# Kernel tuning notes

Measured on AMD Instinct MI355X. Metric: run time of the kernel, lower is better.

The kernel has to match this reference:

```python
import jax, jax.numpy as jnp
import numpy as np

B, N, D, H = 128, 32768, 768, 16
DH = D // H          # per-head hidden_size = memory_dim // num_heads = 48
BETA = 0.25          # scaling (inverse temperature)
STEPS = 5            # update_steps_max
TOPK = 4


def _ln(x, g, b):
    # torch nn.LayerNorm over last dim (biased variance, eps=1e-5), affine
    m = jnp.mean(x, axis=-1, keepdims=True)
    v = jnp.var(x, axis=-1, keepdims=True)
    return (x - m) * jax.lax.rsqrt(v + 1e-5) * g + b


def _l2norm(x):
    # F.normalize(x, dim=-1): x / max(||x||, 1e-12)
    n = jnp.linalg.norm(x, axis=-1, keepdims=True)
    return x / jnp.maximum(n, 1e-12)


def setup_inputs() -> dict:
    key = jax.random.key(0)
    ks = jax.random.split(key, 8)
    s = 0.05  # weight init scale to keep activations sane
    return {
        "query_embedding": jax.random.normal(ks[0], (B, D), jnp.float32),
        "memory_bank": jax.random.normal(ks[1], (N, D), jnp.float32),
        "ln_k_g": jnp.ones((D,), jnp.float32), "ln_k_b": jnp.zeros((D,), jnp.float32),
        "ln_q_g": jnp.ones((D,), jnp.float32), "ln_q_b": jnp.zeros((D,), jnp.float32),
        "ln_v_g": jnp.ones((D,), jnp.float32), "ln_v_b": jnp.zeros((D,), jnp.float32),
        "Wq": jax.random.normal(ks[2], (D, D), jnp.float32) * s, "bq": jnp.zeros((D,), jnp.float32),
        "Wk": jax.random.normal(ks[3], (D, D), jnp.float32) * s, "bk": jnp.zeros((D,), jnp.float32),
        "Wv": jax.random.normal(ks[4], (D, D), jnp.float32) * s, "bv": jnp.zeros((D,), jnp.float32),
        "Wo": jax.random.normal(ks[5], (D, D), jnp.float32) * s, "bo": jnp.zeros((D,), jnp.float32),
        "W1": jax.random.normal(ks[6], (D, D), jnp.float32) * s, "b1": jnp.zeros((D,), jnp.float32),
        "W2": jax.random.normal(ks[7], (D, D), jnp.float32) * s, "b2": jnp.zeros((D,), jnp.float32),
    }


def reference(query_embedding, memory_bank, ln_k_g, ln_k_b, ln_q_g, ln_q_b,
              ln_v_g, ln_v_b, Wq, bq, Wk, bk, Wv, bv, Wo, bo, W1, b1, W2, b2):
    # Affine LayerNorms on stored pattern, state pattern, pattern projection.
    # memory_bank is shared across the batch, so normalize/project it ONCE
    # instead of materializing the (B, N, D) expand from the torch code.
    stored = _ln(memory_bank, ln_k_g, ln_k_b)        # (N, D)
    state = _ln(query_embedding, ln_q_g, ln_q_b)     # (B, D) -- state pattern, seq len 1
    projp = _ln(memory_bank, ln_v_g, ln_v_b)         # (N, D)

    k = (stored @ Wk.T + bk).reshape(N, H, DH)       # (N, H, dh)
    v = (projp @ Wv.T + bv).reshape(N, H, DH)        # (N, H, dh)
    q = (state @ Wq.T + bq).reshape(B, H, DH)        # (B, H, dh)

    # Hopfield convergence: xi <- softmax(beta * xi K^T) K, repeated STEPS times
    def step(xi, _):
        attn = jax.nn.softmax(BETA * jnp.einsum('bhd,nhd->bhn', xi, k), axis=-1)
        return jnp.einsum('bhn,nhd->bhd', attn, k), None

    xi, _ = jax.lax.scan(step, q, None, length=STEPS)

    # Final readout against the (separately normalized) pattern projection V
    attn = jax.nn.softmax(BETA * jnp.einsum('bhd,nhd->bhn', xi, k), axis=-1)  # (B, H, N)
    converged = jnp.einsum('bhn,nhd->bhd', attn, v).reshape(B, D) @ Wo.T + bo  # (B, D)

    # Retrieval head: residual + MLP + cosine-sim logits + top-k
    combined = query_embedding + converged
    rq = jax.nn.relu(combined @ W1.T + b1) @ W2.T + b2
    logits = (_l2norm(rq) @ _l2norm(memory_bank).T) * 20.0   # (B, N)
    top_indices = jax.lax.top_k(logits, TOPK)[1]              # (B, TOPK)
    return top_indices, logits
```

## Files before the change

kernel.cpp:

```cpp
#include <hip/hip_runtime.h>
#include <math.h>

#define NTOT 32768
#define DMODEL 768
#define BSZ 128
#define NHEAD 16
#define DH 48
#define BETA 0.25f

typedef _Float16 f16;
typedef f16 f16x8 __attribute__((ext_vector_type(8)));
typedef f16 f16x4 __attribute__((ext_vector_type(4)));
typedef float f32x4 __attribute__((ext_vector_type(4)));

__global__ __launch_bounds__(256)
void row_stats(const float* __restrict__ X, int M, float* __restrict__ mean,
               float* __restrict__ rstd, float* __restrict__ l2inv) {
  const int row = blockIdx.x * 4 + (threadIdx.x >> 6);
  const int lane = threadIdx.x & 63;
  if (row >= M) return;
  const float* x = X + (size_t)row * DMODEL;
  float s = 0.f, s2 = 0.f;
  for (int i = lane; i < DMODEL; i += 64) {
    float v = x[i];
    s += v; s2 += v * v;
  }
#pragma unroll
  for (int off = 32; off; off >>= 1) {
    s  += __shfl_xor(s, off);
    s2 += __shfl_xor(s2, off);
  }
  if (lane == 0) {
    float mu = s * (1.f / DMODEL);
    float var = s2 * (1.f / DMODEL) - mu * mu;
    mean[row] = mu;
    rstd[row] = rsqrtf(var + 1e-5f);
    if (l2inv) l2inv[row] = 1.f / fmaxf(sqrtf(s2), 1e-12f);
  }
}

__global__ __launch_bounds__(256)
void stats_norm_mb(const float* __restrict__ mb, f16* __restrict__ nh_hi,
                   f16* __restrict__ nh_lo, float* __restrict__ c1,
                   float* __restrict__ c2) {
  const int row = blockIdx.x * 4 + (threadIdx.x >> 6);
  const int lane = threadIdx.x & 63;
  const float* x = mb + (size_t)row * DMODEL;
  float v[12];
  float s = 0.f, s2 = 0.f;
#pragma unroll
  for (int j = 0; j < 3; j++) {
    const float4 v4 = *(const float4*)(x + lane * 4 + j * 256);
    v[j * 4 + 0] = v4.x; v[j * 4 + 1] = v4.y;
    v[j * 4 + 2] = v4.z; v[j * 4 + 3] = v4.w;
    s += v4.x + v4.y + v4.z + v4.w;
    s2 += v4.x * v4.x + v4.y * v4.y + v4.z * v4.z + v4.w * v4.w;
  }
#pragma unroll
  for (int off = 32; off; off >>= 1) {
    s  += __shfl_xor(s, off);
    s2 += __shfl_xor(s2, off);
  }
  const float mu = s * (1.f / DMODEL);
  const float var = s2 * (1.f / DMODEL) - mu * mu;
  const float istd = sqrtf(var + 1e-5f);
  const float rs = 1.f / istd;
  f16* oh = nh_hi + (size_t)row * DMODEL;
  f16* ol = nh_lo + (size_t)row * DMODEL;
#pragma unroll
  for (int j = 0; j < 3; j++) {
    f16x4 h4, l4;
#pragma unroll
    for (int q = 0; q < 4; q++) {
      const float sv = (v[j * 4 + q] - mu) * rs;
      const f16 h = (f16)sv;
      h4[q] = h;
      l4[q] = (f16)(sv - (float)h);
    }
    *(f16x4*)(oh + lane * 4 + j * 256) = h4;
    *(f16x4*)(ol + lane * 4 + j * 256) = l4;
  }
  if (lane == 0) {
    const float l2i = 1.f / fmaxf(sqrtf(s2), 1e-12f);
    c1[row] = 20.f * l2i * istd;
    c2[row] = 20.f * l2i * mu;
  }
}

__global__ __launch_bounds__(256)
void rq_prep(const float* __restrict__ rq, f16* __restrict__ hi,
             f16* __restrict__ lo, float* __restrict__ ainv,
             float* __restrict__ rqsum) {
  const int row = blockIdx.x * 4 + (threadIdx.x >> 6);
  const int lane = threadIdx.x & 63;
  const float* x = rq + (size_t)row * DMODEL;
  f16* oh = hi + (size_t)row * DMODEL;
  f16* ol = lo + (size_t)row * DMODEL;
  float s = 0.f, s2 = 0.f;
#pragma unroll
  for (int j = 0; j < 3; j++) {
    const int d = lane * 4 + j * 256;
    const float4 v4 = *(const float4*)(x + d);
    const float vv[4] = {v4.x, v4.y, v4.z, v4.w};
    f16x4 h4, l4;
#pragma unroll
    for (int q = 0; q < 4; q++) {
      s += vv[q]; s2 += vv[q] * vv[q];
      const f16 h = (f16)vv[q];
      h4[q] = h;
      l4[q] = (f16)(vv[q] - (float)h);
    }
    *(f16x4*)(oh + d) = h4;
    *(f16x4*)(ol + d) = l4;
  }
#pragma unroll
  for (int off = 32; off; off >>= 1) {
    s  += __shfl_xor(s, off);
    s2 += __shfl_xor(s2, off);
  }
  if (lane == 0) {
    rqsum[row] = s;
    ainv[row] = 1.f / fmaxf(sqrtf(s2), 1e-12f);
  }
}

__global__ __launch_bounds__(256)
void prep_w(const float* __restrict__ Wk, const float* __restrict__ bk,
            const float* __restrict__ gk, const float* __restrict__ blnk,
            const float* __restrict__ Wv, const float* __restrict__ bv,
            const float* __restrict__ gv, const float* __restrict__ blnv,
            f16* __restrict__ Wc_hi, f16* __restrict__ Wc_lo,
            float* __restrict__ biasc) {
  const int o = blockIdx.x * 4 + (threadIdx.x >> 6);
  const int lane = threadIdx.x & 63;
  const bool isK = o < DMODEL;
  const float* W = isK ? (Wk + (size_t)o * DMODEL)
                       : (Wv + (size_t)(o - DMODEL) * DMODEL);
  const float* g   = isK ? gk : gv;
  const float* bln = isK ? blnk : blnv;
  float bacc = 0.f;
  for (int d = lane * 4; d < DMODEL; d += 256) {
    const float4 wv = *(const float4*)(W + d);
    const float4 g4 = *(const float4*)(g + d);
    const float4 b4 = *(const float4*)(bln + d);
    bacc += wv.x * b4.x + wv.y * b4.y + wv.z * b4.z + wv.w * b4.w;
    const float sv[4] = {wv.x * g4.x * 16.f, wv.y * g4.y * 16.f,
                         wv.z * g4.z * 16.f, wv.w * g4.w * 16.f};
    f16x4 h4, l4;
#pragma unroll
    for (int j = 0; j < 4; j++) {
      const f16 h = (f16)sv[j];
      h4[j] = h;
      l4[j] = (f16)(sv[j] - (float)h);
    }
    *(f16x4*)(Wc_hi + (size_t)o * DMODEL + d) = h4;
    *(f16x4*)(Wc_lo + (size_t)o * DMODEL + d) = l4;
  }
#pragma unroll
  for (int off = 32; off; off >>= 1) bacc += __shfl_xor(bacc, off);
  if (lane == 0) biasc[o] = (isK ? bk[o] : bv[o - DMODEL]) + bacc;
}

__global__ __launch_bounds__(256)
void proj_mfma(const f16* __restrict__ nh_hi, const f16* __restrict__ nh_lo,
               const f16* __restrict__ Wc_hi, const f16* __restrict__ Wc_lo,
               const float* __restrict__ biasc,
               f16* __restrict__ k_hi, f16* __restrict__ k_lo,
               f16* __restrict__ T_hi, f16* __restrict__ T_lo, int oc0) {
  __shared__ __align__(16) f16 As[128][64];
  __shared__ __align__(16) f16 Bs[128][64];
  const int t = threadIdx.x;
  const int n0 = oc0 + blockIdx.x * 128;
  const int m0 = blockIdx.y * 128;
  const int w = t >> 6, lane = t & 63;
  const int l15 = lane & 15, lq = lane >> 4;
  const int wm = w >> 1, wn = w & 1;
  const int sc = (lane & 7) ^ (lane >> 3);
  const int srow = lane >> 3;

  f32x4 acc[4][4];
#pragma unroll
  for (int a = 0; a < 4; a++)
#pragma unroll
    for (int b = 0; b < 4; b++)
#pragma unroll
      for (int r = 0; r < 4; r++) acc[a][b][r] = 0.f;

  for (int k0 = 0; k0 < DMODEL; k0 += 32) {
    __syncthreads();
#pragma unroll
    for (int i = 0; i < 4; i++) {
      const int rb = (w * 4 + i) * 8;
      const f16* asrc = ((sc < 4) ? nh_hi : nh_lo) +
          (size_t)(m0 + rb + srow) * DMODEL + k0 + (sc & 3) * 8;
      __builtin_amdgcn_global_load_lds(
          (__attribute__((address_space(1))) void*)asrc,
          (__attribute__((address_space(3))) void*)&As[rb][0], 16, 0, 0);
      const f16* bsrc = ((sc < 4) ? Wc_hi : Wc_lo) +
          (size_t)(n0 + rb + srow) * DMODEL + k0 + (sc & 3) * 8;
      __builtin_amdgcn_global_load_lds(
          (__attribute__((address_space(1))) void*)bsrc,
          (__attribute__((address_space(3))) void*)&Bs[rb][0], 16, 0, 0);
    }
    __syncthreads();

    f16x8 nhh[4], nhl[4];
#pragma unroll
    for (int fm = 0; fm < 4; fm++) {
      const int row = wm * 64 + fm * 16 + l15;
      const int e = row & 7;
      nhh[fm] = *(const f16x8*)&As[row][(lq ^ e) * 8];
      nhl[fm] = *(const f16x8*)&As[row][((lq + 4) ^ e) * 8];
    }
    f16x8 wh[4], wl[4];
#pragma unroll
    for (int fo = 0; fo < 4; fo++) {
      const int row = wn * 64 + fo * 16 + l15;
      const int e = row & 7;
      wh[fo] = *(const f16x8*)&Bs[row][(lq ^ e) * 8];
      wl[fo] = *(const f16x8*)&Bs[row][((lq + 4) ^ e) * 8];
    }
#pragma unroll
    for (int fo = 0; fo < 4; fo++)
#pragma unroll
      for (int fm = 0; fm < 4; fm++) {
        f32x4 a = acc[fo][fm];
        a = __builtin_amdgcn_mfma_f32_16x16x32_f16(wh[fo], nhh[fm], a, 0, 0, 0);
        a = __builtin_amdgcn_mfma_f32_16x16x32_f16(wh[fo], nhl[fm], a, 0, 0, 0);
        a = __builtin_amdgcn_mfma_f32_16x16x32_f16(wl[fo], nhh[fm], a, 0, 0, 0);
        acc[fo][fm] = a;
      }
  }
  const int oc = n0 + wn * 64;
  const int obase = (oc - oc0) + lq * 4;
  const bool wantRow = (oc0 == 0);
#pragma unroll
  for (int fo = 0; fo < 4; fo++) {
    const float4 bb = *(const float4*)(biasc + oc + fo * 16 + lq * 4);
    const float bbv[4] = {bb.x, bb.y, bb.z, bb.w};
    const int o = obase + fo * 16;
#pragma unroll
    for (int fm = 0; fm < 4; fm++) {
      const int mrow = m0 + wm * 64 + fm * 16 + l15;
      f16x4 h4, l4;
#pragma unroll
      for (int r = 0; r < 4; r++) {
        const float v = acc[fo][fm][r] * 0.0625f + bbv[r];
        const f16 h = (f16)v;
        h4[r] = h;
        l4[r] = (f16)(v - (float)h);
      }
      if (wantRow) {
        const size_t moff = (size_t)mrow * DMODEL + o;
        *(f16x4*)(k_hi + moff) = h4;
        *(f16x4*)(k_lo + moff) = l4;
      }
#pragma unroll
      for (int r = 0; r < 4; r++) {
        T_hi[(size_t)(o + r) * NTOT + mrow] = h4[r];
        T_lo[(size_t)(o + r) * NTOT + mrow] = l4[r];
      }
    }
  }
}

__global__ __launch_bounds__(256)
void logits_mfma(const f16* __restrict__ nh_hi, const f16* __restrict__ nh_lo,
                 const f16* __restrict__ rq_hi, const f16* __restrict__ rq_lo,
                 const float* __restrict__ c1, const float* __restrict__ c2,
                 const float* __restrict__ ainv, const float* __restrict__ rqsum,
                 float* __restrict__ out) {
  __shared__ __align__(16) f16 As[128][64];
  __shared__ __align__(16) f16 Bs[128][64];
  const int t = threadIdx.x;
  const int n0 = blockIdx.x * 128;
  const int w = t >> 6, lane = t & 63;
  const int l15 = lane & 15, lq = lane >> 4;
  const int wm = w >> 1, wn = w & 1;
  const int sc = (lane & 7) ^ (lane >> 3);
  const int srow = lane >> 3;

  f32x4 acc[4][4];
#pragma unroll
  for (int a = 0; a < 4; a++)
#pragma unroll
    for (int b = 0; b < 4; b++)
#pragma unroll
      for (int r = 0; r < 4; r++) acc[a][b][r] = 0.f;

  for (int k0 = 0; k0 < DMODEL; k0 += 32) {
    __syncthreads();
#pragma unroll
    for (int i = 0; i < 4; i++) {
      const int rb = (w * 4 + i) * 8;
      const f16* asrc = ((sc < 4) ? nh_hi : nh_lo) +
          (size_t)(n0 + rb + srow) * DMODEL + k0 + (sc & 3) * 8;
      __builtin_amdgcn_global_load_lds(
          (__attribute__((address_space(1))) void*)asrc,
          (__attribute__((address_space(3))) void*)&As[rb][0], 16, 0, 0);
      const f16* bsrc = ((sc < 4) ? rq_hi : rq_lo) +
          (size_t)(rb + srow) * DMODEL + k0 + (sc & 3) * 8;
      __builtin_amdgcn_global_load_lds(
          (__attribute__((address_space(1))) void*)bsrc,
          (__attribute__((address_space(3))) void*)&Bs[rb][0], 16, 0, 0);
    }
    __syncthreads();

    f16x8 ah[4], al[4];
#pragma unroll
    for (int fo = 0; fo < 4; fo++) {
      const int row = wn * 64 + fo * 16 + l15;
      const int e = row & 7;
      ah[fo] = *(const f16x8*)&As[row][(lq ^ e) * 8];
      al[fo] = *(const f16x8*)&As[row][((lq + 4) ^ e) * 8];
    }
    f16x8 bh[4], bl[4];
#pragma unroll
    for (int fm = 0; fm < 4; fm++) {
      const int row = wm * 64 + fm * 16 + l15;
      const int e = row & 7;
      bh[fm] = *(const f16x8*)&Bs[row][(lq ^ e) * 8];
      bl[fm] = *(const f16x8*)&Bs[row][((lq + 4) ^ e) * 8];
    }
#pragma unroll
    for (int fo = 0; fo < 4; fo++)
#pragma unroll
      for (int fm = 0; fm < 4; fm++) {
        f32x4 a = acc[fo][fm];
        a = __builtin_amdgcn_mfma_f32_16x16x32_f16(ah[fo], bh[fm], a, 0, 0, 0);
        a = __builtin_amdgcn_mfma_f32_16x16x32_f16(ah[fo], bl[fm], a, 0, 0, 0);
        a = __builtin_amdgcn_mfma_f32_16x16x32_f16(al[fo], bh[fm], a, 0, 0, 0);
        acc[fo][fm] = a;
      }
  }
#pragma unroll
  for (int fm = 0; fm < 4; fm++) {
    const int b = wm * 64 + fm * 16 + l15;
    const float am = ainv[b];
    const float rs = rqsum[b];
#pragma unroll
    for (int fo = 0; fo < 4; fo++) {
      const int nb = n0 + wn * 64 + fo * 16 + lq * 4;
      const float4 c1v = *(const float4*)(c1 + nb);
      const float4 c2v = *(const float4*)(c2 + nb);
      const float c1a[4] = {c1v.x, c1v.y, c1v.z, c1v.w};
      const float c2a[4] = {c2v.x, c2v.y, c2v.z, c2v.w};
      float4 o4;
      float ov[4];
#pragma unroll
      for (int r = 0; r < 4; r++)
        ov[r] = am * (acc[fo][fm][r] * c1a[r] + rs * c2a[r]);
      o4.x = ov[0]; o4.y = ov[1]; o4.z = ov[2]; o4.w = ov[3];
      *(float4*)(out + (size_t)b * NTOT + nb) = o4;
    }
  }
}

__global__ __launch_bounds__(256)
void ln_gemm_f32(const float* __restrict__ A, const float* __restrict__ mean,
                 const float* __restrict__ rstd, const float* __restrict__ g,
                 const float* __restrict__ bln, const float* __restrict__ W,
                 const float* __restrict__ bias, float* __restrict__ out) {
  __shared__ float As[16][68];
  __shared__ float Ws[16][68];
  const int t = threadIdx.x;
  const int m0 = blockIdx.y << 6, n0 = blockIdx.x << 6;
  const int tm = t >> 4, tn = t & 15;
  const int lr = t >> 2;
  const int lk = (t & 3) << 2;
  const float muL = mean[m0 + lr];
  const float rsL = rstd[m0 + lr];
  float acc[4][4] = {};
  for (int k0 = 0; k0 < DMODEL; k0 += 16) {
    float4 a4 = *(const float4*)(A + (size_t)(m0 + lr) * DMODEL + k0 + lk);
    float4 g4 = *(const float4*)(g + k0 + lk);
    float4 b4 = *(const float4*)(bln + k0 + lk);
    As[lk + 0][lr] = (a4.x - muL) * rsL * g4.x + b4.x;
    As[lk + 1][lr] = (a4.y - muL) * rsL * g4.y + b4.y;
    As[lk + 2][lr] = (a4.z - muL) * rsL * g4.z + b4.z;
    As[lk + 3][lr] = (a4.w - muL) * rsL * g4.w + b4.w;
    float4 w4 = *(const float4*)(W + (size_t)(n0 + lr) * DMODEL + k0 + lk);
    Ws[lk + 0][lr] = w4.x;
    Ws[lk + 1][lr] = w4.y;
    Ws[lk + 2][lr] = w4.z;
    Ws[lk + 3][lr] = w4.w;
    __syncthreads();
#pragma unroll
    for (int kk = 0; kk < 16; kk++) {
      const float4 av = *(const float4*)(&As[kk][tm * 4]);
      const float4 bv = *(const float4*)(&Ws[kk][tn * 4]);
      const float a[4] = {av.x, av.y, av.z, av.w};
      const float b[4] = {bv.x, bv.y, bv.z, bv.w};
#pragma unroll
      for (int i = 0; i < 4; i++)
#pragma unroll
        for (int j = 0; j < 4; j++) acc[i][j] += a[i] * b[j];
    }
    __syncthreads();
  }
  const float4 bia = *(const float4*)(bias + n0 + tn * 4);
  const float bb[4] = {bia.x, bia.y, bia.z, bia.w};
#pragma unroll
  for (int i = 0; i < 4; i++) {
    const int m = m0 + tm * 4 + i;
    float4 o4;
    o4.x = acc[i][0] + bb[0];
    o4.y = acc[i][1] + bb[1];
    o4.z = acc[i][2] + bb[2];
    o4.w = acc[i][3] + bb[3];
    *(float4*)(out + (size_t)m * DMODEL + n0 + tn * 4) = o4;
  }
}

__global__ __launch_bounds__(256)
void gemm_bias(const float* __restrict__ A, const float* __restrict__ W,
               const float* __restrict__ bias, const float* __restrict__ add,
               float* __restrict__ out, int relu) {
  __shared__ float As[16][68];
  __shared__ float Ws[16][68];
  const int t = threadIdx.x;
  const int m0 = blockIdx.y << 6, n0 = blockIdx.x << 6;
  const int tm = t >> 4, tn = t & 15;
  const int lr = t >> 2;
  const int lk = (t & 3) << 2;
  float acc[4][4] = {};
  for (int k0 = 0; k0 < DMODEL; k0 += 16) {
    float4 a4 = *(const float4*)(A + (size_t)(m0 + lr) * DMODEL + k0 + lk);
    As[lk + 0][lr] = a4.x;
    As[lk + 1][lr] = a4.y;
    As[lk + 2][lr] = a4.z;
    As[lk + 3][lr] = a4.w;
    float4 w4 = *(const float4*)(W + (size_t)(n0 + lr) * DMODEL + k0 + lk);
    Ws[lk + 0][lr] = w4.x;
    Ws[lk + 1][lr] = w4.y;
    Ws[lk + 2][lr] = w4.z;
    Ws[lk + 3][lr] = w4.w;
    __syncthreads();
#pragma unroll
    for (int kk = 0; kk < 16; kk++) {
      const float4 av = *(const float4*)(&As[kk][tm * 4]);
      const float4 bv = *(const float4*)(&Ws[kk][tn * 4]);
      const float a[4] = {av.x, av.y, av.z, av.w};
      const float b[4] = {bv.x, bv.y, bv.z, bv.w};
#pragma unroll
      for (int i = 0; i < 4; i++)
#pragma unroll
        for (int j = 0; j < 4; j++) acc[i][j] += a[i] * b[j];
    }
    __syncthreads();
  }
  const float4 bia = *(const float4*)(bias + n0 + tn * 4);
  const float bb[4] = {bia.x, bia.y, bia.z, bia.w};
#pragma unroll
  for (int i = 0; i < 4; i++) {
    const int m = m0 + tm * 4 + i;
    float v[4];
#pragma unroll
    for (int j = 0; j < 4; j++) v[j] = acc[i][j] + bb[j];
    if (add) {
      const float4 a4 = *(const float4*)(add + (size_t)m * DMODEL + n0 + tn * 4);
      v[0] += a4.x; v[1] += a4.y; v[2] += a4.z; v[3] += a4.w;
    }
    if (relu) {
#pragma unroll
      for (int j = 0; j < 4; j++) v[j] = fmaxf(v[j], 0.f);
    }
    float4 o4 = {v[0], v[1], v[2], v[3]};
    *(float4*)(out + (size_t)m * DMODEL + n0 + tn * 4) = o4;
  }
}

__global__ __launch_bounds__(256)
void split_xi_k(const float* __restrict__ xi, f16* __restrict__ hi,
                f16* __restrict__ lo) {
  const int i = blockIdx.x * 256 + threadIdx.x;
  float4 v = ((const float4*)xi)[i];
  float s[4] = {v.x * BETA, v.y * BETA, v.z * BETA, v.w * BETA};
  f16x4 h4, l4;
#pragma unroll
  for (int j = 0; j < 4; j++) {
    f16 h = (f16)s[j];
    h4[j] = h;
    l4[j] = (f16)(s[j] - (float)h);
  }
  ((f16x4*)hi)[i] = h4;
  ((f16x4*)lo)[i] = l4;
}

#define FCHUNK 64
#define FROWS (NTOT / FCHUNK)

__global__ __launch_bounds__(256)
void flash_round(const f16* __restrict__ k_hi, const f16* __restrict__ k_lo,
                 const f16* __restrict__ pvT_hi, const f16* __restrict__ pvT_lo,
                 const f16* __restrict__ xi_hi, const f16* __restrict__ xi_lo,
                 float* __restrict__ part_ml, float* __restrict__ part_o) {
  const int h = blockIdx.y, chunk = blockIdx.x;
  const int tid = threadIdx.x, w = tid >> 6, lane = tid & 63;
  const int l15 = lane & 15, lq = lane >> 4;
  const int b0 = w * 32;

  __shared__ __align__(16) f16 krow[2][32][56];
  __shared__ __align__(16) f16 ptT[2][48][40];
  __shared__ __align__(16) f16 pHi[4][32][40];
  __shared__ __align__(16) f16 pLo[4][32][40];

  const int nbase = chunk * FROWS;

  const f16* ssrc[3];
  f16* sdst[3];
  int sstep[3];
#pragma unroll
  for (int cc = 0; cc < 3; cc++) {
    const int idx = cc * 256 + tid;
    if (idx < 384) {
      const int tsel = idx / 192, q = idx % 192;
      const int r = q / 6, c = q % 6;
      ssrc[cc] = (tsel ? k_lo : k_hi) + (size_t)(nbase + r) * DMODEL + h * DH + c * 8;
      sdst[cc] = &krow[tsel][r][c * 8];
      sstep[cc] = 32 * DMODEL;
    } else {
      const int j = idx - 384;
      const int tsel = j / 192, q = j % 192;
      const int d = q / 4, c = q % 4;
      ssrc[cc] = (tsel ? pvT_lo : pvT_hi) + (size_t)(h * DH + d) * NTOT + nbase + c * 8;
      sdst[cc] = &ptT[tsel][d][c * 8];
      sstep[cc] = 32;
    }
  }

  const f16x8 zf = {};
  f16x8 xqh[2][2], xql[2][2];
#pragma unroll
  for (int bt = 0; bt < 2; bt++) {
    const size_t xoff = (size_t)(b0 + bt * 16 + l15) * DMODEL + h * DH;
    xqh[bt][0] = *(const f16x8*)(xi_hi + xoff + lq * 8);
    xql[bt][0] = *(const f16x8*)(xi_lo + xoff + lq * 8);
    const size_t xo1 = xoff + 32 + (lq & 1) * 8;
    f16x8 th = *(const f16x8*)(xi_hi + xo1);
    f16x8 tl = *(const f16x8*)(xi_lo + xo1);
    xqh[bt][1] = (lq < 2) ? th : zf;
    xql[bt][1] = (lq < 2) ? tl : zf;
  }

  float m[2] = {-1e30f, -1e30f}, lsum[2] = {0.f, 0.f};
  f32x4 O[3][2];
#pragma unroll
  for (int mt = 0; mt < 3; mt++)
#pragma unroll
    for (int bt = 0; bt < 2; bt++)
#pragma unroll
      for (int j = 0; j < 4; j++) O[mt][bt][j] = 0.f;

  f16x8 stg[3];
#pragma unroll
  for (int cc = 0; cc < 3; cc++) {
    stg[cc] = *(const f16x8*)ssrc[cc];
    ssrc[cc] += sstep[cc];
  }
#pragma unroll
  for (int cc = 0; cc < 3; cc++) *(f16x8*)sdst[cc] = stg[cc];
  __syncthreads();

  for (int it = 0; it < 16; it++) {
    if (it < 15) {
#pragma unroll
      for (int cc = 0; cc < 3; cc++) {
        stg[cc] = *(const f16x8*)ssrc[cc];
        ssrc[cc] += sstep[cc];
      }
    }

    f16x8 akh[2][2], akl[2][2];
#pragma unroll
    for (int nt = 0; nt < 2; nt++) {
      const int row = nt * 16 + l15;
      akh[nt][0] = *(const f16x8*)&krow[0][row][lq * 8];
      akl[nt][0] = *(const f16x8*)&krow[1][row][lq * 8];
      f16x8 t0 = *(const f16x8*)&krow[0][row][32 + (lq & 1) * 8];
      f16x8 t1 = *(const f16x8*)&krow[1][row][32 + (lq & 1) * 8];
      akh[nt][1] = (lq < 2) ? t0 : zf;
      akl[nt][1] = (lq < 2) ? t1 : zf;
    }
    f32x4 S[2][2];
#pragma unroll
    for (int nt = 0; nt < 2; nt++)
#pragma unroll
      for (int bt = 0; bt < 2; bt++) {
        f32x4 s = {};
        s = __builtin_amdgcn_mfma_f32_16x16x32_f16(akh[nt][0], xqh[bt][0], s, 0, 0, 0);
        s = __builtin_amdgcn_mfma_f32_16x16x32_f16(akh[nt][1], xqh[bt][1], s, 0, 0, 0);
        s = __builtin_amdgcn_mfma_f32_16x16x32_f16(akh[nt][0], xql[bt][0], s, 0, 0, 0);
        s = __builtin_amdgcn_mfma_f32_16x16x32_f16(akh[nt][1], xql[bt][1], s, 0, 0, 0);
        s = __builtin_amdgcn_mfma_f32_16x16x32_f16(akl[nt][0], xqh[bt][0], s, 0, 0, 0);
        s = __builtin_amdgcn_mfma_f32_16x16x32_f16(akl[nt][1], xqh[bt][1], s, 0, 0, 0);
        S[nt][bt] = s;
      }
    float sc[2];
#pragma unroll
    for (int bt = 0; bt < 2; bt++) {
      float mx = S[0][bt][0];
#pragma unroll
      for (int r = 1; r < 4; r++) mx = fmaxf(mx, S[0][bt][r]);
#pragma unroll
      for (int r = 0; r < 4; r++) mx = fmaxf(mx, S[1][bt][r]);
      mx = fmaxf(mx, __shfl_xor(mx, 16));
      mx = fmaxf(mx, __shfl_xor(mx, 32));
      const float mnew = fmaxf(m[bt], mx);
      sc[bt] = __expf(m[bt] - mnew);
      float ps = 0.f;
#pragma unroll
      for (int nt = 0; nt < 2; nt++) {
        f16x4 ph, pl;
#pragma unroll
        for (int r = 0; r < 4; r++) {
          const float p = __expf(S[nt][bt][r] - mnew);
          ps += p;
          const f16 hh = (f16)p;
          ph[r] = hh;
          pl[r] = (f16)(p - (float)hh);
        }
        *(f16x4*)&pHi[w][bt * 16 + l15][nt * 16 + lq * 4] = ph;
        *(f16x4*)&pLo[w][bt * 16 + l15][nt * 16 + lq * 4] = pl;
      }
      ps += __shfl_xor(ps, 16);
      ps += __shfl_xor(ps, 32);
      lsum[bt] = lsum[bt] * sc[bt] + ps;
      m[bt] = mnew;
    }
    __asm__ volatile("s_waitcnt lgkmcnt(0)" ::: "memory");
    f16x8 avh[3], avl[3];
#pragma unroll
    for (int mt = 0; mt < 3; mt++) {
      avh[mt] = *(const f16x8*)&ptT[0][mt * 16 + l15][lq * 8];
      avl[mt] = *(const f16x8*)&ptT[1][mt * 16 + l15][lq * 8];
    }
    f16x8 pbh[2], pbl[2];
#pragma unroll
    for (int bt = 0; bt < 2; bt++) {
      pbh[bt] = *(const f16x8*)&pHi[w][bt * 16 + l15][lq * 8];
      pbl[bt] = *(const f16x8*)&pLo[w][bt * 16 + l15][lq * 8];
    }
#pragma unroll
    for (int mt = 0; mt < 3; mt++)
#pragma unroll
      for (int bt = 0; bt < 2; bt++) {
#pragma unroll
        for (int j = 0; j < 4; j++) O[mt][bt][j] *= sc[bt];
        f32x4 o = O[mt][bt];
        o = __builtin_amdgcn_mfma_f32_16x16x32_f16(avh[mt], pbh[bt], o, 0, 0, 0);
        o = __builtin_amdgcn_mfma_f32_16x16x32_f16(avh[mt], pbl[bt], o, 0, 0, 0);
        o = __builtin_amdgcn_mfma_f32_16x16x32_f16(avl[mt], pbh[bt], o, 0, 0, 0);
        O[mt][bt] = o;
      }

    if (it < 15) {
      __syncthreads();
#pragma unroll
      for (int cc = 0; cc < 3; cc++) *(f16x8*)sdst[cc] = stg[cc];
      __syncthreads();
    }
  }
  const int pc = h * FCHUNK + chunk;
  if (lq == 0) {
#pragma unroll
    for (int bt = 0; bt < 2; bt++) {
      float* pm = part_ml + ((size_t)pc * BSZ + b0 + bt * 16 + l15) * 2;
      pm[0] = m[bt];
      pm[1] = lsum[bt];
    }
  }
#pragma unroll
  for (int mt = 0; mt < 3; mt++)
#pragma unroll
    for (int bt = 0; bt < 2; bt++) {
      float* po = part_o + ((size_t)pc * BSZ + b0 + bt * 16 + l15) * 48 +
                  mt * 16 + lq * 4;
      *(f32x4*)po = O[mt][bt];
    }
}

__global__ __launch_bounds__(64)
void hopfield_combine(const float* __restrict__ part_ml,
                      const float* __restrict__ part_o, float* __restrict__ dst) {
  const int bh = blockIdx.x;
  const int h = bh >> 7, b = bh & 127;
  const int c = threadIdx.x;
  __shared__ float w[64];
  const float* pm = part_ml + ((size_t)(h * 64 + c) * BSZ + b) * 2;
  const float mp = pm[0];
  const float lp = pm[1];
  float M = mp;
#pragma unroll
  for (int off = 32; off; off >>= 1) M = fmaxf(M, __shfl_xor(M, off));
  const float wp = __expf(mp - M);
  w[c] = wp;
  float L = lp * wp;
#pragma unroll
  for (int off = 32; off; off >>= 1) L += __shfl_xor(L, off);
  __syncthreads();
  if (c < DH) {
    float o = 0.f;
    for (int p = 0; p < 64; p++)
      o += part_o[((size_t)(h * 64 + p) * BSZ + b) * 48 + c] * w[p];
    dst[(size_t)b * DMODEL + h * DH + c] = o / L;
  }
}

__global__ __launch_bounds__(256)
void topk_kernel(const float* __restrict__ logits, float* __restrict__ outIdx) {
  const int b = blockIdx.x;
  const int t = threadIdx.x;
  const float* row = logits + (size_t)b * NTOT;
  float v[4] = {-1e30f, -1e30f, -1e30f, -1e30f};
  int id[4] = {0x7fffffff, 0x7fffffff, 0x7fffffff, 0x7fffffff};
  for (int n = t; n < NTOT; n += 256) {
    const float x = row[n];
    if (x > v[3]) {
      v[3] = x; id[3] = n;
#pragma unroll
      for (int s = 3; s > 0; s--) {
        const bool sw = (v[s] > v[s - 1]) || (v[s] == v[s - 1] && id[s] < id[s - 1]);
        if (sw) {
          float tv = v[s]; v[s] = v[s - 1]; v[s - 1] = tv;
          int ti = id[s]; id[s] = id[s - 1]; id[s - 1] = ti;
        }
      }
    }
  }
  __shared__ float sv[256][4];
  __shared__ int si[256][4];
#pragma unroll
  for (int j = 0; j < 4; j++) { sv[t][j] = v[j]; si[t][j] = id[j]; }
  for (int str = 128; str >= 1; str >>= 1) {
    __syncthreads();
    if (t < str) {
      float a[4], c[4];
      int ai[4], ci[4];
#pragma unroll
      for (int j = 0; j < 4; j++) {
        a[j] = sv[t][j]; ai[j] = si[t][j];
        c[j] = sv[t + str][j]; ci[j] = si[t + str][j];
      }
      float rv[4]; int ri[4];
      int p = 0, q = 0;
#pragma unroll
      for (int oo = 0; oo < 4; oo++) {
        const bool ta = (a[p] > c[q]) || (a[p] == c[q] && ai[p] < ci[q]);
        if (ta) { rv[oo] = a[p]; ri[oo] = ai[p]; p++; }
        else    { rv[oo] = c[q]; ri[oo] = ci[q]; q++; }
      }
#pragma unroll
      for (int j = 0; j < 4; j++) { sv[t][j] = rv[j]; si[t][j] = ri[j]; }
    }
  }
  if (t == 0) {
#pragma unroll
    for (int j = 0; j < 4; j++) outIdx[b * 4 + j] = (float)si[0][j];
  }
}

extern "C" void kernel_launch(void* const* d_in, const int* in_sizes, int n_in,
                              void* d_out, int out_size, void* d_ws, size_t ws_size,
                              hipStream_t stream) {
  const float* qe    = (const float*)d_in[0];
  const float* mb    = (const float*)d_in[1];
  const float* ln_kg = (const float*)d_in[2];
  const float* ln_kb = (const float*)d_in[3];
  const float* ln_qg = (const float*)d_in[4];
  const float* ln_qb = (const float*)d_in[5];
  const float* ln_vg = (const float*)d_in[6];
  const float* ln_vb = (const float*)d_in[7];
  const float* Wq = (const float*)d_in[8];
  const float* bq = (const float*)d_in[9];
  const float* Wk = (const float*)d_in[10];
  const float* bk = (const float*)d_in[11];
  const float* Wv = (const float*)d_in[12];
  const float* bv = (const float*)d_in[13];
  const float* Wo = (const float*)d_in[14];
  const float* bo = (const float*)d_in[15];
  const float* W1 = (const float*)d_in[16];
  const float* b1 = (const float*)d_in[17];
  const float* W2 = (const float*)d_in[18];
  const float* b2 = (const float*)d_in[19];

  float* out = (float*)d_out;
  float* logits = out + BSZ * 4;

  float* ws = (float*)d_ws;
  size_t off = 0;
  auto alloc = [&](size_t n) { float* p = ws + off; off += n; return p; };
  const size_t ND2 = (size_t)NTOT * DMODEL / 2;
  float* c1      = alloc(NTOT);
  float* c2      = alloc(NTOT);
  float* q_mean  = alloc(128);
  float* q_rstd  = alloc(128);
  float* rq_inv  = alloc(128);
  float* rq_sum  = alloc(128);
  float* pad_    = alloc(256);
  f16* k_hi  = (f16*)alloc(ND2);
  f16* k_lo  = (f16*)alloc(ND2);
  f16* T_hi  = (f16*)alloc(ND2);
  f16* T_lo  = (f16*)alloc(ND2);
  f16* nh_hi = (f16*)alloc(ND2);
  f16* nh_lo = (f16*)alloc(ND2);
  float* part_ml = alloc((size_t)NHEAD * FCHUNK * BSZ * 2);
  float* part_o  = alloc((size_t)NHEAD * FCHUNK * BSZ * 48);
  float* xi   = alloc((size_t)BSZ * DMODEL);
  float* conv = alloc((size_t)BSZ * DMODEL);
  float* comb = alloc((size_t)BSZ * DMODEL);
  float* h1   = alloc((size_t)BSZ * DMODEL);
  f16* xi_hi = (f16*)alloc((size_t)BSZ * DMODEL / 2);
  f16* xi_lo = (f16*)alloc((size_t)BSZ * DMODEL / 2);
  f16* rq_hi = (f16*)alloc((size_t)BSZ * DMODEL / 2);
  f16* rq_lo = (f16*)alloc((size_t)BSZ * DMODEL / 2);
  f16* Wc_hi = (f16*)alloc((size_t)2 * DMODEL * DMODEL / 2);
  f16* Wc_lo = (f16*)alloc((size_t)2 * DMODEL * DMODEL / 2);
  float* biasc = alloc(2 * DMODEL);
  (void)ws_size; (void)in_sizes; (void)n_in; (void)out_size; (void)pad_;

  row_stats<<<BSZ / 4, 256, 0, stream>>>(qe, BSZ, q_mean, q_rstd, nullptr);
  stats_norm_mb<<<NTOT / 4, 256, 0, stream>>>(mb, nh_hi, nh_lo, c1, c2);
  prep_w<<<2 * DMODEL / 4, 256, 0, stream>>>(Wk, bk, ln_kg, ln_kb,
                                             Wv, bv, ln_vg, ln_vb,
                                             Wc_hi, Wc_lo, biasc);

  proj_mfma<<<dim3(DMODEL / 128, NTOT / 128), 256, 0, stream>>>(
      nh_hi, nh_lo, Wc_hi, Wc_lo, biasc, k_hi, k_lo, T_hi, T_lo, 0);
  ln_gemm_f32<<<dim3(DMODEL / 64, BSZ / 64), 256, 0, stream>>>(
      qe, q_mean, q_rstd, ln_qg, ln_qb, Wq, bq, xi);

  for (int r = 0; r < 5; r++) {
    split_xi_k<<<96, 256, 0, stream>>>(xi, xi_hi, xi_lo);
    flash_round<<<dim3(FCHUNK, NHEAD), 256, 0, stream>>>(
        k_hi, k_lo, T_hi, T_lo, xi_hi, xi_lo, part_ml, part_o);
    hopfield_combine<<<BSZ * NHEAD, 64, 0, stream>>>(part_ml, part_o, xi);
  }

  proj_mfma<<<dim3(DMODEL / 128, NTOT / 128), 256, 0, stream>>>(
      nh_hi, nh_lo, Wc_hi, Wc_lo, biasc, k_hi, k_lo, T_hi, T_lo, DMODEL);

  split_xi_k<<<96, 256, 0, stream>>>(xi, xi_hi, xi_lo);
  flash_round<<<dim3(FCHUNK, NHEAD), 256, 0, stream>>>(
      k_hi, k_lo, T_hi, T_lo, xi_hi, xi_lo, part_ml, part_o);
  hopfield_combine<<<BSZ * NHEAD, 64, 0, stream>>>(part_ml, part_o, conv);

  gemm_bias<<<dim3(DMODEL / 64, BSZ / 64), 256, 0, stream>>>(conv, Wo, bo, qe, comb, 0);
  gemm_bias<<<dim3(DMODEL / 64, BSZ / 64), 256, 0, stream>>>(comb, W1, b1, nullptr, h1, 1);
  float* rq = conv;
  gemm_bias<<<dim3(DMODEL / 64, BSZ / 64), 256, 0, stream>>>(h1, W2, b2, nullptr, rq, 0);

  rq_prep<<<BSZ / 4, 256, 0, stream>>>(rq, rq_hi, rq_lo, rq_inv, rq_sum);
  logits_mfma<<<NTOT / 128, 256, 0, stream>>>(nh_hi, nh_lo, rq_hi, rq_lo,
                                              c1, c2, rq_inv, rq_sum, logits);

  topk_kernel<<<BSZ, 256, 0, stream>>>(logits, out);
}
```

Measured before the change: 1.309 ms.

## Double-buffer flash tiles via direct global-to-LDS loads and swizzle proj grid

The flash_round kernel now stages K and transposed-V tiles with global_load_lds straight into a double-buffered LDS region. This removes the register round-trip and one barrier per iteration, and lets the next tile's load overlap compute. The V tile uses an XOR swizzle on the LDS layout to avoid bank conflicts, since padding is no longer possible. proj_mfma also remaps workgroup IDs with an 8-way swizzle for better L2 locality. LDS usage grows and correctness depends on load completion ordering at the single remaining barrier.

```diff
diff --git a/kernel.cpp b/kernel.cpp
--- a/kernel.cpp
+++ b/kernel.cpp
@@ -170,8 +170,12 @@
   __shared__ __align__(16) f16 As[128][64];
   __shared__ __align__(16) f16 Bs[128][64];
   const int t = threadIdx.x;
-  const int n0 = oc0 + blockIdx.x * 128;
-  const int m0 = blockIdx.y * 128;
+  const int nwg = gridDim.x * gridDim.y;
+  const int bid = blockIdx.x + blockIdx.y * gridDim.x;
+  const int swz = (bid & 7) * (nwg >> 3) + (bid >> 3);
+  const int bx = swz % gridDim.x, by = swz / gridDim.x;
+  const int n0 = oc0 + bx * 128;
+  const int m0 = by * 128;
   const int w = t >> 6, lane = t & 63;
   const int l15 = lane & 15, lq = lane >> 4;
   const int wm = w >> 1, wn = w & 1;
@@ -500,32 +504,30 @@
   const int l15 = lane & 15, lq = lane >> 4;
   const int b0 = w * 32;
 
-  __shared__ __align__(16) f16 krow[2][32][56];
-  __shared__ __align__(16) f16 ptT[2][48][40];
+  __shared__ __align__(16) f16 stage[2][6144];
   __shared__ __align__(16) f16 pHi[4][32][40];
   __shared__ __align__(16) f16 pLo[4][32][40];
 
   const int nbase = chunk * FROWS;
 
-  const f16* ssrc[3];
-  f16* sdst[3];
-  int sstep[3];
-#pragma unroll
-  for (int cc = 0; cc < 3; cc++) {
-    const int idx = cc * 256 + tid;
-    if (idx < 384) {
-      const int tsel = idx / 192, q = idx % 192;
-      const int r = q / 6, c = q % 6;
-      ssrc[cc] = (tsel ? k_lo : k_hi) + (size_t)(nbase + r) * DMODEL + h * DH + c * 8;
-      sdst[cc] = &krow[tsel][r][c * 8];
-      sstep[cc] = 32 * DMODEL;
+  const f16* gsrc[3];
+  int gstep[3];
+#pragma unroll
+  for (int g = 0; g < 3; g++) {
+    const int s = w * 3 + g;
+    const int ci = s * 64 + lane;
+    if (s < 6) {
+      const int tsel = ci / 192, rem = ci % 192;
+      const int r = rem / 6, dc = rem % 6;
+      gsrc[g] = (tsel ? k_lo : k_hi) + (size_t)(nbase + r) * DMODEL + h * DH + dc * 8;
+      gstep[g] = 32 * DMODEL;
     } else {
-      const int j = idx - 384;
-      const int tsel = j / 192, q = j % 192;
-      const int d = q / 4, c = q % 4;
-      ssrc[cc] = (tsel ? pvT_lo : pvT_hi) + (size_t)(h * DH + d) * NTOT + nbase + c * 8;
-      sdst[cc] = &ptT[tsel][d][c * 8];
-      sstep[cc] = 32;
+      const int j = ci - 384;
+      const int tsel = j / 192, rem = j % 192;
+      const int d = rem / 4, pc = rem % 4;
+      const int nc = pc ^ (d & 3);
+      gsrc[g] = (tsel ? pvT_lo : pvT_hi) + (size_t)(h * DH + d) * NTOT + nbase + nc * 8;
+      gstep[g] = 32;
     }
   }
 
@@ -552,33 +554,38 @@
 #pragma unroll
       for (int j = 0; j < 4; j++) O[mt][bt][j] = 0.f;
 
-  f16x8 stg[3];
-#pragma unroll
-  for (int cc = 0; cc < 3; cc++) {
-    stg[cc] = *(const f16x8*)ssrc[cc];
-    ssrc[cc] += sstep[cc];
-  }
-#pragma unroll
-  for (int cc = 0; cc < 3; cc++) *(f16x8*)sdst[cc] = stg[cc];
+#pragma unroll
+  for (int g = 0; g < 3; g++) {
+    __builtin_amdgcn_global_load_lds(
+        (__attribute__((address_space(1))) void*)gsrc[g],
+        (__attribute__((address_space(3))) void*)&stage[0][(w * 3 + g) * 512],
+        16, 0, 0);
+    gsrc[g] += gstep[g];
+  }
   __syncthreads();
 
+  int cur = 0;
   for (int it = 0; it < 16; it++) {
     if (it < 15) {
 #pragma unroll
-      for (int cc = 0; cc < 3; cc++) {
-        stg[cc] = *(const f16x8*)ssrc[cc];
-        ssrc[cc] += sstep[cc];
-      }
-    }
+      for (int g = 0; g < 3; g++) {
+        __builtin_amdgcn_global_load_lds(
+            (__attribute__((address_space(1))) void*)gsrc[g],
+            (__attribute__((address_space(3))) void*)&stage[cur ^ 1][(w * 3 + g) * 512],
+            16, 0, 0);
+        gsrc[g] += gstep[g];
+      }
+    }
+    const f16* st = stage[cur];
 
     f16x8 akh[2][2], akl[2][2];
 #pragma unroll
     for (int nt = 0; nt < 2; nt++) {
       const int row = nt * 16 + l15;
-      akh[nt][0] = *(const f16x8*)&krow[0][row][lq * 8];
-      akl[nt][0] = *(const f16x8*)&krow[1][row][lq * 8];
-      f16x8 t0 = *(const f16x8*)&krow[0][row][32 + (lq & 1) * 8];
-      f16x8 t1 = *(const f16x8*)&krow[1][row][32 + (lq & 1) * 8];
+      akh[nt][0] = *(const f16x8*)&st[row * 48 + lq * 8];
+      akl[nt][0] = *(const f16x8*)&st[1536 + row * 48 + lq * 8];
+      f16x8 t0 = *(const f16x8*)&st[row * 48 + 32 + (lq & 1) * 8];
+      f16x8 t1 = *(const f16x8*)&st[1536 + row * 48 + 32 + (lq & 1) * 8];
       akh[nt][1] = (lq < 2) ? t0 : zf;
       akl[nt][1] = (lq < 2) ? t1 : zf;
     }
@@ -632,8 +639,10 @@
     f16x8 avh[3], avl[3];
 #pragma unroll
     for (int mt = 0; mt < 3; mt++) {
-      avh[mt] = *(const f16x8*)&ptT[0][mt * 16 + l15][lq * 8];
-      avl[mt] = *(const f16x8*)&ptT[1][mt * 16 + l15][lq * 8];
+      const int d = mt * 16 + l15;
+      const int po = (lq ^ (d & 3)) * 8;
+      avh[mt] = *(const f16x8*)&st[3072 + d * 32 + po];
+      avl[mt] = *(const f16x8*)&st[3072 + 1536 + d * 32 + po];
     }
     f16x8 pbh[2], pbl[2];
 #pragma unroll
@@ -656,9 +665,7 @@
 
     if (it < 15) {
       __syncthreads();
-#pragma unroll
-      for (int cc = 0; cc < 3; cc++) *(f16x8*)sdst[cc] = stg[cc];
-      __syncthreads();
+      cur ^= 1;
     }
   }
   const int pc = h * FCHUNK + chunk;
```

Result: slower. 1.377 ms (+5.2%).
